# Optimization experiments

Measured on AMD Instinct MI355X. Metric: run time of the kernel, lower is better.

Reference implementation:

```python
import jax, jax.numpy as jnp
import numpy as np

N_FEATS = 9       # OGB atom feature columns
VOCAB = 119       # per-feature embedding vocab (max OGB atom vocab)
HIDDEN = 128
NUM_HEADS = 8
HEAD_DIM = HIDDEN // NUM_HEADS


def setup_inputs() -> dict:
    key = jax.random.key(0)
    ks = jax.random.split(key, 12)
    N, K = 50000, 16
    X = jax.random.randint(ks[0], (N, N_FEATS), 0, VOCAB)
    nbr_idx = jax.random.randint(ks[1], (N, K), 0, N)
    nbr_mask = jax.random.randint(ks[2], (N, K), 0, 2).astype(bool)
    atom_emb = jax.random.normal(ks[3], (N_FEATS, VOCAB, HIDDEN), jnp.float32) * 0.02
    s = 1.0 / np.sqrt(HIDDEN)
    Wq = jax.random.normal(ks[4], (HIDDEN, HIDDEN), jnp.float32) * s
    bq = jnp.zeros((HIDDEN,), jnp.float32)
    Wk = jax.random.normal(ks[5], (HIDDEN, HIDDEN), jnp.float32) * s
    bk = jnp.zeros((HIDDEN,), jnp.float32)
    Wv = jax.random.normal(ks[6], (HIDDEN, HIDDEN), jnp.float32) * s
    bv = jnp.zeros((HIDDEN,), jnp.float32)
    return {"X": X, "nbr_idx": nbr_idx, "nbr_mask": nbr_mask,
            "atom_emb": atom_emb, "Wq": Wq, "bq": bq,
            "Wk": Wk, "bk": bk, "Wv": Wv, "bv": bv}


def reference(X, nbr_idx, nbr_mask, atom_emb, Wq, bq, Wk, bk, Wv, bv):
    N = X.shape[0]
    # AtomEncoder: sum per-feature embedding lookups -> [N, HIDDEN]
    h = jnp.sum(atom_emb[jnp.arange(N_FEATS)[None, :], X], axis=1)
    scaling = HEAD_DIM ** -0.5
    q = (h @ Wq + bq).reshape(N, NUM_HEADS, HEAD_DIM) * scaling
    k = (h @ Wk + bk).reshape(N, NUM_HEADS, HEAD_DIM)
    v = (h @ Wv + bv).reshape(N, NUM_HEADS, HEAD_DIM)
    # ELL-format sparse attention: gather padded neighbor k/v -> [N, K, H, D]
    k_n = k[nbr_idx]
    v_n = v[nbr_idx]
    scores = jnp.einsum('nhd,nkhd->nkh', q, k_n)          # [N, K, H]
    scores = jnp.where(nbr_mask[..., None], scores, -1e9)
    attn = jax.nn.softmax(scores, axis=1)                 # softmax over neighbors
    out = jnp.einsum('nkh,nkhd->nhd', attn, v_n)          # [N, H, D]
    return out.reshape(N, HIDDEN)
```

## Files before the change

kernel.cpp:

```cpp
#include <hip/hip_runtime.h>
#include <hip/hip_bf16.h>

#define NFEAT 9
#define VOCAB 119
#define HIDDEN 128
#define NHEAD 8
#define HDIM 16
#define KNBR 16

typedef __attribute__((ext_vector_type(8))) short short8;
typedef __attribute__((ext_vector_type(4))) float f32x4;

__device__ __forceinline__ void load_lds16(const void* g, void* l) {
    __builtin_amdgcn_global_load_lds((const __attribute__((address_space(1))) void*)g,
                                     (__attribute__((address_space(3))) void*)l, 16, 0, 0);
}

__global__ void fill_kernel(float* out, int n, float val) {
    int i = blockIdx.x * blockDim.x + threadIdx.x;
    if (i < n) out[i] = val;
}

__global__ __launch_bounds__(256) void wt_kernel(
    const float* __restrict__ Wq, const float* __restrict__ Wk,
    const float* __restrict__ Wv, short* __restrict__ Wt)
{
    int mat = blockIdx.x >> 2, tile = blockIdx.x & 3;
    const float* W = (mat == 0) ? Wq : (mat == 1) ? Wk : Wv;
    __shared__ float ls[32 * HIDDEN];
    int tid = threadIdx.x;
    int cc0 = tile * 32;
    #pragma unroll
    for (int j = 0; j < 16; ++j) {
        int idx = j * 256 + tid;
        ls[idx] = W[(size_t)cc0 * HIDDEN + idx];
    }
    __syncthreads();
    int c = tid & 127, hf = tid >> 7;
    unsigned int ob[8];
    #pragma unroll
    for (int j = 0; j < 8; ++j) {
        int ccl = hf * 16 + 2 * j;
        __hip_bfloat16 b0 = __float2bfloat16(ls[ccl * HIDDEN + c]);
        __hip_bfloat16 b1 = __float2bfloat16(ls[(ccl + 1) * HIDDEN + c]);
        ob[j] = (unsigned int)*reinterpret_cast<unsigned short*>(&b0)
              | ((unsigned int)*reinterpret_cast<unsigned short*>(&b1) << 16);
    }
    unsigned int* dst = reinterpret_cast<unsigned int*>(
        Wt + (size_t)mat * HIDDEN * HIDDEN + (size_t)c * HIDDEN + cc0 + hf * 16);
    #pragma unroll
    for (int j = 0; j < 8; ++j) dst[j] = ob[j];
}

#define MT 64
#define HBS 136

__global__ __launch_bounds__(256) void qkv_kernel(
    const int* __restrict__ X, const float* __restrict__ emb,
    const short* __restrict__ Wt,
    const float* __restrict__ bq, const float* __restrict__ bk,
    const float* __restrict__ bv,
    float* __restrict__ qf, __hip_bfloat16* __restrict__ kv, int N)
{
    __shared__ __align__(16) short hb[MT * HBS];
    __shared__ int xs[MT * NFEAT];

    const int tid = threadIdx.x;
    const int n0 = blockIdx.x * MT;

    for (int i = tid; i < MT * NFEAT; i += 256) {
        int n = n0 + i / NFEAT;
        int v = (n < N) ? X[(size_t)n * NFEAT + (i % NFEAT)] : 0;
        xs[i] = min(max(v, 0), VOCAB - 1);
    }
    __syncthreads();

    {
        const int cg = tid & 31;
        const int slot = tid >> 5;
        #pragma unroll
        for (int i = 0; i < 8; ++i) {
            int nl = slot * 8 + i;
            float4 acc = {0.f, 0.f, 0.f, 0.f};
            #pragma unroll
            for (int f = 0; f < NFEAT; ++f) {
                const float4 e = *reinterpret_cast<const float4*>(
                    &emb[((size_t)f * VOCAB + xs[nl * NFEAT + f]) * HIDDEN + cg * 4]);
                acc.x += e.x; acc.y += e.y; acc.z += e.z; acc.w += e.w;
            }
            __hip_bfloat162 p0 = __float22bfloat162_rn(make_float2(acc.x, acc.y));
            __hip_bfloat162 p1 = __float22bfloat162_rn(make_float2(acc.z, acc.w));
            uint2 u;
            u.x = *reinterpret_cast<unsigned int*>(&p0);
            u.y = *reinterpret_cast<unsigned int*>(&p1);
            *reinterpret_cast<uint2*>(&hb[nl * HBS + cg * 4]) = u;
        }
    }
    __syncthreads();

    const int wave = tid >> 6, lane = tid & 63;
    const int l15 = lane & 15, quad = lane >> 4;
    const int mloc = wave * 16 + l15;

    short8 a[4];
    #pragma unroll
    for (int k0 = 0; k0 < 4; ++k0)
        a[k0] = *reinterpret_cast<const short8*>(&hb[mloc * HBS + k0 * 32 + quad * 8]);

    #pragma unroll
    for (int mat = 0; mat < 3; ++mat) {
        const short* Wm = Wt + (size_t)mat * HIDDEN * HIDDEN;
        const float* bias = (mat == 0) ? bq : (mat == 1) ? bk : bv;
        #pragma unroll
        for (int nt = 0; nt < 8; ++nt) {
            f32x4 acc = {0.f, 0.f, 0.f, 0.f};
            int n = nt * 16 + l15;
            #pragma unroll
            for (int k0 = 0; k0 < 4; ++k0) {
                short8 b = *reinterpret_cast<const short8*>(
                    &Wm[n * HIDDEN + k0 * 32 + quad * 8]);
                acc = __builtin_amdgcn_mfma_f32_16x16x32_bf16(a[k0], b, acc, 0, 0, 0);
            }
            float bb = bias[n];
            #pragma unroll
            for (int r = 0; r < 4; ++r) {
                int node = n0 + wave * 16 + quad * 4 + r;
                if (node < N) {
                    float val = acc[r] + bb;
                    if (mat == 0)      qf[(size_t)node * HIDDEN + n] = val * 0.25f;
                    else if (mat == 1) kv[(size_t)node * 256 + n] = __float2bfloat16(val);
                    else               kv[(size_t)node * 256 + 128 + n] = __float2bfloat16(val);
                }
            }
        }
    }
}

#define NPB2 2

__global__ __launch_bounds__(256) void attn_kernel(
    const int* __restrict__ nbr_idx, const int* __restrict__ nbr_mask,
    const float* __restrict__ qf, const __hip_bfloat16* __restrict__ kv,
    float* __restrict__ out, int N)
{
    __shared__ __align__(16) __hip_bfloat16 kvl[NPB2][KNBR][256];
    __shared__ float ql[NPB2][HIDDEN];
    __shared__ float sl[NPB2][KNBR][NHEAD + 1];
    __shared__ float el[NPB2][KNBR][NHEAD + 1];
    __shared__ int idxl[NPB2][KNBR];
    __shared__ int mskl[NPB2][KNBR];

    const int tid = threadIdx.x;
    const int local = tid >> 7;
    const int t = tid & 127;
    int n = blockIdx.x * NPB2 + local;
    if (n >= N) n = N - 1;

    ql[local][t] = qf[(size_t)n * HIDDEN + t];
    if (t < KNBR) {
        int iv = nbr_idx[(size_t)n * KNBR + t];
        idxl[local][t] = min(max(iv, 0), N - 1);
        mskl[local][t] = nbr_mask[(size_t)n * KNBR + t];
    }
    __syncthreads();

    {
        const int w2 = t >> 6;
        const int l = t & 63;
        #pragma unroll
        for (int j = 0; j < 4; ++j) {
            int r = 4 * j + 2 * w2 + (l >> 5);
            const short* src = (const short*)kv
                + (size_t)idxl[local][r] * 256 + (size_t)(l & 31) * 8;
            load_lds16(src, &kvl[local][4 * j + 2 * w2][0]);
        }
    }
    __syncthreads();

    const int kk = t >> 3, hh = t & 7;
    float s = 0.f;
    {
        const __hip_bfloat162* kp =
            reinterpret_cast<const __hip_bfloat162*>(&kvl[local][kk][hh * HDIM]);
        const float* qp = &ql[local][hh * HDIM];
        #pragma unroll
        for (int d2 = 0; d2 < HDIM / 2; ++d2) {
            float2 kf = __bfloat1622float2(kp[d2]);
            s += qp[2 * d2] * kf.x + qp[2 * d2 + 1] * kf.y;
        }
    }
    if (!mskl[local][kk]) s = -1e9f;
    sl[local][kk][hh] = s;
    __syncthreads();

    float mx = -3.0e38f;
    #pragma unroll
    for (int j = 0; j < KNBR; ++j) mx = fmaxf(mx, sl[local][j][hh]);
    float e = __expf(s - mx);
    el[local][kk][hh] = e;
    __syncthreads();
    float denom = 0.f;
    #pragma unroll
    for (int j = 0; j < KNBR; ++j) denom += el[local][j][hh];
    sl[local][kk][hh] = e / denom;
    __syncthreads();

    const int h2 = t >> 4, dd = t & 15;
    float o = 0.f;
    #pragma unroll
    for (int j = 0; j < KNBR; ++j) {
        float a = sl[local][j][h2];
        float vv = __bfloat162float(kvl[local][j][HIDDEN + h2 * HDIM + dd]);
        o += a * vv;
    }
    out[(size_t)n * HIDDEN + t] = o;
}

extern "C" void kernel_launch(void* const* d_in, const int* in_sizes, int n_in,
                              void* d_out, int out_size, void* d_ws, size_t ws_size,
                              hipStream_t stream)
{
    float* out = (float*)d_out;

    bool ok = (n_in == 10);
    int N = ok ? in_sizes[0] / NFEAT : 0;
    ok = ok && N > 0 && in_sizes[0] == N * NFEAT
            && in_sizes[1] == N * KNBR
            && in_sizes[2] == N * KNBR
            && in_sizes[3] == NFEAT * VOCAB * HIDDEN
            && in_sizes[4] == HIDDEN * HIDDEN && in_sizes[5] == HIDDEN
            && in_sizes[6] == HIDDEN * HIDDEN && in_sizes[7] == HIDDEN
            && in_sizes[8] == HIDDEN * HIDDEN && in_sizes[9] == HIDDEN
            && out_size == N * HIDDEN;
    if (!ok) {
        fill_kernel<<<(out_size + 255) / 256, 256, 0, stream>>>(out, out_size, 0.0f);
        return;
    }
    size_t need = (size_t)N * 1024 + 3 * HIDDEN * HIDDEN * sizeof(short);
    if (ws_size < need) {
        fill_kernel<<<(out_size + 255) / 256, 256, 0, stream>>>(out, out_size, 1.0f);
        return;
    }

    const int* X        = (const int*)d_in[0];
    const int* nbr_idx  = (const int*)d_in[1];
    const int* nbr_mask = (const int*)d_in[2];
    const float* emb = (const float*)d_in[3];
    const float* Wq  = (const float*)d_in[4];
    const float* bq  = (const float*)d_in[5];
    const float* Wk  = (const float*)d_in[6];
    const float* bk  = (const float*)d_in[7];
    const float* Wv  = (const float*)d_in[8];
    const float* bv  = (const float*)d_in[9];

    float* qf = (float*)d_ws;
    __hip_bfloat16* kv =
        (__hip_bfloat16*)((char*)d_ws + (size_t)N * HIDDEN * sizeof(float));
    short* Wt = (short*)((char*)d_ws + (size_t)N * 1024);

    wt_kernel<<<12, 256, 0, stream>>>(Wq, Wk, Wv, Wt);
    qkv_kernel<<<(N + MT - 1) / MT, 256, 0, stream>>>(
        X, emb, Wt, bq, bk, bv, qf, kv, N);
    attn_kernel<<<(N + NPB2 - 1) / NPB2, 256, 0, stream>>>(
        nbr_idx, nbr_mask, qf, kv, out, N);
}
```

Baseline: 200.4 us.

## Halve QKV tile rows and split output columns across waves with batched weight loads

```diff
diff --git a/kernel.cpp b/kernel.cpp
--- a/kernel.cpp
+++ b/kernel.cpp
@@ -52,10 +52,10 @@
     for (int j = 0; j < 8; ++j) dst[j] = ob[j];
 }
 
-#define MT 64
+#define MT 32
 #define HBS 136
 
-__global__ __launch_bounds__(256) void qkv_kernel(
+__global__ __launch_bounds__(256, 4) void qkv_kernel(
     const int* __restrict__ X, const float* __restrict__ emb,
     const short* __restrict__ Wt,
     const float* __restrict__ bq, const float* __restrict__ bk,
@@ -79,8 +79,8 @@
         const int cg = tid & 31;
         const int slot = tid >> 5;
         #pragma unroll
-        for (int i = 0; i < 8; ++i) {
-            int nl = slot * 8 + i;
+        for (int i = 0; i < 4; ++i) {
+            int nl = slot * 4 + i;
             float4 acc = {0.f, 0.f, 0.f, 0.f};
             #pragma unroll
             for (int f = 0; f < NFEAT; ++f) {
@@ -100,7 +100,8 @@
 
     const int wave = tid >> 6, lane = tid & 63;
     const int l15 = lane & 15, quad = lane >> 4;
-    const int mloc = wave * 16 + l15;
+    const int mtile = wave & 1, nthalf = wave >> 1;
+    const int mloc = mtile * 16 + l15;
 
     short8 a[4];
     #pragma unroll
@@ -108,25 +109,31 @@
         a[k0] = *reinterpret_cast<const short8*>(&hb[mloc * HBS + k0 * 32 + quad * 8]);
 
     #pragma unroll
-    for (int mat = 0; mat < 3; ++mat) {
-        const short* Wm = Wt + (size_t)mat * HIDDEN * HIDDEN;
-        const float* bias = (mat == 0) ? bq : (mat == 1) ? bk : bv;
-        #pragma unroll
-        for (int nt = 0; nt < 8; ++nt) {
-            f32x4 acc = {0.f, 0.f, 0.f, 0.f};
-            int n = nt * 16 + l15;
-            #pragma unroll
-            for (int k0 = 0; k0 < 4; ++k0) {
-                short8 b = *reinterpret_cast<const short8*>(
-                    &Wm[n * HIDDEN + k0 * 32 + quad * 8]);
-                acc = __builtin_amdgcn_mfma_f32_16x16x32_bf16(a[k0], b, acc, 0, 0, 0);
-            }
-            float bb = bias[n];
+    for (int nt = 0; nt < 4; ++nt) {
+        const int ntg = nthalf * 4 + nt;
+        const int n = ntg * 16 + l15;
+        short8 b[3][4];
+        #pragma unroll
+        for (int mat = 0; mat < 3; ++mat)
+            #pragma unroll
+            for (int k0 = 0; k0 < 4; ++k0)
+                b[mat][k0] = *reinterpret_cast<const short8*>(
+                    &Wt[(size_t)mat * HIDDEN * HIDDEN + n * HIDDEN + k0 * 32 + quad * 8]);
+        f32x4 acc[3] = {{0.f,0.f,0.f,0.f},{0.f,0.f,0.f,0.f},{0.f,0.f,0.f,0.f}};
+        #pragma unroll
+        for (int mat = 0; mat < 3; ++mat)
+            #pragma unroll
+            for (int k0 = 0; k0 < 4; ++k0)
+                acc[mat] = __builtin_amdgcn_mfma_f32_16x16x32_bf16(
+                    a[k0], b[mat][k0], acc[mat], 0, 0, 0);
+        float bb[3] = {bq[n], bk[n], bv[n]};
+        #pragma unroll
+        for (int mat = 0; mat < 3; ++mat) {
             #pragma unroll
             for (int r = 0; r < 4; ++r) {
-                int node = n0 + wave * 16 + quad * 4 + r;
+                int node = n0 + mtile * 16 + quad * 4 + r;
                 if (node < N) {
-                    float val = acc[r] + bb;
+                    float val = acc[mat][r] + bb[mat];
                     if (mat == 0)      qf[(size_t)node * HIDDEN + n] = val * 0.25f;
                     else if (mat == 1) kv[(size_t)node * 256 + n] = __float2bfloat16(val);
                     else               kv[(size_t)node * 256 + 128 + n] = __float2bfloat16(val);
```

After: 196.1 us. 2.1% less time.
